# Kernel tuning notes

Measured on AMD Instinct MI355X. Metric: run time of the kernel, lower is better.

## Reference

```python
import jax, jax.numpy as jnp
import numpy as np

B, S, D, H, BLK = 2, 2048, 1024, 16, 128
DH = D // H
NB = S // BLK
EPS = 1e-5
NEG = -1e9


def _make_layout():
    i = np.arange(NB)[:, None]
    j = np.arange(NB)[None, :]
    # causal: local block diagonal + previous block + global first block column
    lay = ((j == i) | (j == i - 1) | (j == 0)) & (j <= i)
    return jnp.asarray(np.broadcast_to(lay, (H, NB, NB)).astype(np.int32))


def setup_inputs() -> dict:
    key = jax.random.key(0)
    ks = jax.random.split(key, 8)
    sd = 1.0 / np.sqrt(D)
    inp = {
        "x": jax.random.normal(ks[0], (B, S, D), jnp.float32),
        "ln1_g": jnp.ones((D,), jnp.float32),
        "ln1_b": jnp.zeros((D,), jnp.float32),
        "Wq": jax.random.normal(ks[1], (D, D), jnp.float32) * sd,
        "bq": jnp.zeros((D,), jnp.float32),
        "Wk": jax.random.normal(ks[2], (D, D), jnp.float32) * sd,
        "bk": jnp.zeros((D,), jnp.float32),
        "Wv": jax.random.normal(ks[3], (D, D), jnp.float32) * sd,
        "bv": jnp.zeros((D,), jnp.float32),
        "Wo": jax.random.normal(ks[4], (D, D), jnp.float32) * sd,
        "bo": jnp.zeros((D,), jnp.float32),
        "ln2_g": jnp.ones((D,), jnp.float32),
        "ln2_b": jnp.zeros((D,), jnp.float32),
        "W1": jax.random.normal(ks[5], (D, 4 * D), jnp.float32) * sd,
        "b1": jnp.zeros((4 * D,), jnp.float32),
        "W2": jax.random.normal(ks[6], (4 * D, D), jnp.float32) * (1.0 / np.sqrt(4 * D)),
        "b2": jnp.zeros((D,), jnp.float32),
        "layout": _make_layout(),
    }
    return inp


def _ln(x, g, b):
    m = jnp.mean(x, -1, keepdims=True)
    v = jnp.var(x, -1, keepdims=True)
    return (x - m) * jax.lax.rsqrt(v + EPS) * g + b


def reference(x, ln1_g, ln1_b, Wq, bq, Wk, bk, Wv, bv, Wo, bo,
              ln2_g, ln2_b, W1, b1, W2, b2, layout):
    # ---- pre-norm block-sparse multi-head attention + residual ----
    h = _ln(x, ln1_g, ln1_b)
    q = (h @ Wq + bq).reshape(B, S, H, DH).transpose(0, 2, 1, 3)
    k = (h @ Wk + bk).reshape(B, S, H, DH).transpose(0, 2, 1, 3)
    v = (h @ Wv + bv).reshape(B, S, H, DH).transpose(0, 2, 1, 3)

    # expand block layout [H,NB,NB] -> token mask [H,S,S], intersect with causal
    blk_mask = jnp.repeat(jnp.repeat(layout > 0, BLK, axis=1), BLK, axis=2)
    causal = jnp.tril(jnp.ones((S, S), bool))
    mask = blk_mask & causal  # [H,S,S]

    scale = DH ** -0.5
    scores = jnp.einsum("bhqd,bhkd->bhqk", q * scale, k)
    scores = jnp.where(mask[None], scores, NEG)
    att = jax.nn.softmax(scores, axis=-1)
    ctx = jnp.einsum("bhqk,bhkd->bhqd", att, v)
    ctx = ctx.transpose(0, 2, 1, 3).reshape(B, S, D)
    x = x + (ctx @ Wo + bo)

    # ---- pre-norm MLP (GeLU) + residual ----
    h2 = _ln(x, ln2_g, ln2_b)
    ff = jax.nn.gelu(h2 @ W1 + b1, approximate=False) @ W2 + b2
    return x + ff
```

## Files before the change

kernel.cpp:

```cpp
#include <hip/hip_runtime.h>

typedef unsigned short ushort;
typedef unsigned int uint;
typedef __attribute__((ext_vector_type(8))) short short8;
typedef __attribute__((ext_vector_type(4))) float floatx4;

#define DEV __device__ __forceinline__

DEV ushort f2bf(float f) {
    uint u = __float_as_uint(f);
    u += 0x7fffu + ((u >> 16) & 1u);
    return (ushort)(u >> 16);
}

DEV void load_lds16(const void* g, const void* l) {
    __builtin_amdgcn_global_load_lds(
        (const __attribute__((address_space(1))) void*)g,
        (__attribute__((address_space(3))) void*)l, 16, 0, 0);
}

template<int ROWS>
DEV void stage_tile(const ushort* g, int ldg, ushort* lds, int w, int lane) {
#pragma unroll
    for (int t = 0; t < ROWS / 32; ++t) {
        int row = t * 32 + w * 8 + (lane >> 3);
        int cg  = (lane & 7) ^ (row & 7);
        load_lds16(g + (size_t)row * ldg + cg * 8, lds + (t * 32 + w * 8) * 64);
    }
}

DEV short8 frag_ld(const ushort* lds, int row, int ks, int quad) {
    int slot = (ks * 4 + quad) ^ (row & 7);
    return *(const short8*)(lds + row * 64 + slot * 8);
}

__global__ __launch_bounds__(256) void transcvt(const float* __restrict__ in,
                                                ushort* __restrict__ out,
                                                int K, int N) {
    __shared__ float t[64][65];
    int tx = threadIdx.x & 63, ty = threadIdx.x >> 6;
    int k0 = blockIdx.y * 64, n0 = blockIdx.x * 64;
#pragma unroll
    for (int r = ty; r < 64; r += 4)
        t[r][tx] = in[(size_t)(k0 + r) * N + n0 + tx];
    __syncthreads();
#pragma unroll
    for (int r = ty; r < 64; r += 4)
        out[(size_t)(n0 + r) * K + k0 + tx] = f2bf(t[tx][r]);
}

__global__ __launch_bounds__(256) void transcvt4(const float* __restrict__ s0,
                                                 const float* __restrict__ s1,
                                                 const float* __restrict__ s2,
                                                 const float* __restrict__ s3,
                                                 ushort* __restrict__ d0,
                                                 ushort* __restrict__ d1,
                                                 ushort* __restrict__ d2,
                                                 ushort* __restrict__ d3) {
    __shared__ float t[64][65];
    int z = blockIdx.z;
    const float* in = z == 0 ? s0 : (z == 1 ? s1 : (z == 2 ? s2 : s3));
    ushort* out     = z == 0 ? d0 : (z == 1 ? d1 : (z == 2 ? d2 : d3));
    int tx = threadIdx.x & 63, ty = threadIdx.x >> 6;
    int k0 = blockIdx.y * 64, n0 = blockIdx.x * 64;
#pragma unroll
    for (int r = ty; r < 64; r += 4)
        t[r][tx] = in[(size_t)(k0 + r) * 1024 + n0 + tx];
    __syncthreads();
#pragma unroll
    for (int r = ty; r < 64; r += 4)
        out[(size_t)(n0 + r) * 1024 + k0 + tx] = f2bf(t[tx][r]);
}

__global__ __launch_bounds__(256) void bias_concat(const float* __restrict__ bq,
                                                   const float* __restrict__ bk,
                                                   const float* __restrict__ bv,
                                                   float* __restrict__ out) {
    int i = blockIdx.x * 256 + threadIdx.x;
    float v = i < 1024 ? bq[i] : (i < 2048 ? bk[i - 1024] : bv[i - 2048]);
    out[i] = v;
}

__global__ __launch_bounds__(256) void ln_kernel(const float* __restrict__ x,
                                                 const float* __restrict__ g,
                                                 const float* __restrict__ bb,
                                                 ushort* __restrict__ out) {
    int row = blockIdx.x, tid = threadIdx.x;
    float4 v = ((const float4*)(x + (size_t)row * 1024))[tid];
    float s = v.x + v.y + v.z + v.w;
    float q = v.x * v.x + v.y * v.y + v.z * v.z + v.w * v.w;
#pragma unroll
    for (int m = 1; m < 64; m <<= 1) {
        s += __shfl_xor(s, m);
        q += __shfl_xor(q, m);
    }
    __shared__ float ss[4], qs[4];
    int w = tid >> 6;
    if ((tid & 63) == 0) { ss[w] = s; qs[w] = q; }
    __syncthreads();
    s = ss[0] + ss[1] + ss[2] + ss[3];
    q = qs[0] + qs[1] + qs[2] + qs[3];
    float mean = s * (1.0f / 1024.0f);
    float var  = q * (1.0f / 1024.0f) - mean * mean;
    float rs   = rsqrtf(var + 1e-5f);
    float4 gv = ((const float4*)g)[tid];
    float4 bv = ((const float4*)bb)[tid];
    ushort o0 = f2bf((v.x - mean) * rs * gv.x + bv.x);
    ushort o1 = f2bf((v.y - mean) * rs * gv.y + bv.y);
    ushort o2 = f2bf((v.z - mean) * rs * gv.z + bv.z);
    ushort o3 = f2bf((v.w - mean) * rs * gv.w + bv.w);
    uint lo = o0 | ((uint)o1 << 16), hi = o2 | ((uint)o3 << 16);
    ((uint2*)(out + (size_t)row * 1024))[tid] = make_uint2(lo, hi);
}

template<int MODE, int JN>
__global__ __launch_bounds__(256) void gemm128(const ushort* __restrict__ A,
                                               const ushort* __restrict__ Bt,
                                               const float* __restrict__ bias,
                                               const float* __restrict__ res,
                                               void* __restrict__ outp,
                                               int M, int N, int K) {
    constexpr int BN = JN * 32;
    __shared__ ushort As[128 * 64];
    __shared__ ushort Bs[BN * 64];
    int tid = threadIdx.x, w = tid >> 6, lane = tid & 63;
    int quad = lane >> 4, l15 = lane & 15;
    int wm = w >> 1, wn = w & 1;
    int m0 = blockIdx.y * 128, n0 = blockIdx.x * BN;

    floatx4 acc[4][JN] = {};
    for (int k0 = 0; k0 < K; k0 += 64) {
        __syncthreads();
        stage_tile<128>(A + (size_t)m0 * K + k0, K, As, w, lane);
        stage_tile<BN>(Bt + (size_t)n0 * K + k0, K, Bs, w, lane);
        __syncthreads();
#pragma unroll
        for (int ks = 0; ks < 2; ++ks) {
            short8 af[4], bfr[JN];
#pragma unroll
            for (int i = 0; i < 4; ++i) af[i] = frag_ld(As, wm * 64 + i * 16 + l15, ks, quad);
#pragma unroll
            for (int j = 0; j < JN; ++j) bfr[j] = frag_ld(Bs, wn * (JN * 16) + j * 16 + l15, ks, quad);
#pragma unroll
            for (int i = 0; i < 4; ++i)
#pragma unroll
                for (int j = 0; j < JN; ++j)
                    acc[i][j] = __builtin_amdgcn_mfma_f32_16x16x32_bf16(af[i], bfr[j], acc[i][j], 0, 0, 0);
        }
    }
#pragma unroll
    for (int j = 0; j < JN; ++j) {
        int col = n0 + wn * (JN * 16) + j * 16 + l15;
        float bv = bias[col];
#pragma unroll
        for (int i = 0; i < 4; ++i) {
#pragma unroll
            for (int r = 0; r < 4; ++r) {
                int row = m0 + wm * 64 + i * 16 + quad * 4 + r;
                float v = acc[i][j][r] + bv;
                if (MODE == 0) {
                    int which = col >> 10, c2 = col & 1023;
                    int b = row >> 11, s = row & 2047, hh = c2 >> 6, dh = c2 & 63;
                    ((ushort*)outp)[(size_t)which * 4194304 +
                                    (((size_t)(b * 16 + hh)) * 2048 + s) * 64 + dh] = f2bf(v);
                } else if (MODE == 1) {
                    float gl = 0.5f * v * (1.0f + erff(v * 0.70710678118f));
                    ((ushort*)outp)[(size_t)row * N + col] = f2bf(gl);
                } else {
                    ((float*)outp)[(size_t)row * N + col] = res[(size_t)row * N + col] + v;
                }
            }
        }
    }
}

__global__ __launch_bounds__(256) void attn_kernel(const ushort* __restrict__ qg,
                                                   const ushort* __restrict__ kg,
                                                   const ushort* __restrict__ vg,
                                                   ushort* __restrict__ ctx) {
    __shared__ ushort Qs[64 * 64];
    __shared__ ushort Ks[128 * 64];
    __shared__ ushort Vs[64 * 136];
    __shared__ ushort Ps[64 * 136];
    int iq2 = blockIdx.x, h = blockIdx.y, b = blockIdx.z;
    int tid = threadIdx.x, w = tid >> 6, lane = tid & 63;
    int quad = lane >> 4, l15 = lane & 15;
    int iq = iq2 >> 1;

    const ushort* qp    = qg + ((size_t)(b * 16 + h) * 2048 + iq2 * 64) * 64;
    const ushort* kbase = kg + (size_t)(b * 16 + h) * 2048 * 64;
    const ushort* vbase = vg + (size_t)(b * 16 + h) * 2048 * 64;

    stage_tile<64>(qp, 64, Qs, w, lane);

    floatx4 o[4] = {};
    float mi[4], li[4];
#pragma unroll
    for (int r = 0; r < 4; ++r) { mi[r] = -1e30f; li[r] = 0.0f; }

    int jbs[3];
    int nj = 0;
    jbs[nj++] = 0;
    if (iq > 1) jbs[nj++] = iq - 1;
    if (iq > 0) jbs[nj++] = iq;

    for (int ji = 0; ji < nj; ++ji) {
        int jb = jbs[ji];
        __syncthreads();
        stage_tile<128>(kbase + (size_t)jb * 128 * 64, 64, Ks, w, lane);
        {
            int dh = tid & 63, sg = tid >> 6;
            const ushort* vp = vbase + (size_t)jb * 128 * 64;
#pragma unroll
            for (int cc = 0; cc < 8; ++cc) {
                int s0 = sg * 32 + cc * 4;
                ushort e0 = vp[(s0 + 0) * 64 + dh];
                ushort e1 = vp[(s0 + 1) * 64 + dh];
                ushort e2 = vp[(s0 + 2) * 64 + dh];
                ushort e3 = vp[(s0 + 3) * 64 + dh];
                uint lo = e0 | ((uint)e1 << 16), hi = e2 | ((uint)e3 << 16);
                *(uint2*)(Vs + dh * 136 + s0) = make_uint2(lo, hi);
            }
        }
        __syncthreads();

        floatx4 sacc[8] = {};
#pragma unroll
        for (int ks = 0; ks < 2; ++ks) {
            short8 af = frag_ld(Qs, w * 16 + l15, ks, quad);
            short8 bf8[8];
#pragma unroll
            for (int nt = 0; nt < 8; ++nt) bf8[nt] = frag_ld(Ks, nt * 16 + l15, ks, quad);
#pragma unroll
            for (int nt = 0; nt < 8; ++nt)
                sacc[nt] = __builtin_amdgcn_mfma_f32_16x16x32_bf16(af, bf8[nt], sacc[nt], 0, 0, 0);
        }

        float rowmax[4] = {-1e30f, -1e30f, -1e30f, -1e30f};
        bool diag = (jb == iq);
        int rowL0 = (iq2 & 1) * 64 + w * 16 + quad * 4;
#pragma unroll
        for (int nt = 0; nt < 8; ++nt) {
#pragma unroll
            for (int r = 0; r < 4; ++r) {
                float xv = sacc[nt][r] * 0.125f;
                if (diag && (nt * 16 + l15 > rowL0 + r)) xv = -1e30f;
                sacc[nt][r] = xv;
                rowmax[r] = fmaxf(rowmax[r], xv);
            }
        }
#pragma unroll
        for (int r = 0; r < 4; ++r)
#pragma unroll
            for (int m = 1; m < 16; m <<= 1)
                rowmax[r] = fmaxf(rowmax[r], __shfl_xor(rowmax[r], m));

        float alpha[4], rsum[4];
#pragma unroll
        for (int r = 0; r < 4; ++r) {
            float mnew = fmaxf(mi[r], rowmax[r]);
            alpha[r] = __expf(mi[r] - mnew);
            mi[r] = mnew;
            rsum[r] = 0.0f;
        }
#pragma unroll
        for (int nt = 0; nt < 8; ++nt) {
#pragma unroll
            for (int r = 0; r < 4; ++r) {
                float p = __expf(sacc[nt][r] - mi[r]);
                rsum[r] += p;
                Ps[(w * 16 + quad * 4 + r) * 136 + nt * 16 + l15] = f2bf(p);
            }
        }
#pragma unroll
        for (int r = 0; r < 4; ++r) {
#pragma unroll
            for (int m = 1; m < 16; m <<= 1) rsum[r] += __shfl_xor(rsum[r], m);
            li[r] = li[r] * alpha[r] + rsum[r];
        }
#pragma unroll
        for (int nt = 0; nt < 4; ++nt)
#pragma unroll
            for (int r = 0; r < 4; ++r) o[nt][r] *= alpha[r];

#pragma unroll
        for (int ks2 = 0; ks2 < 4; ++ks2) {
            short8 ap = *(const short8*)(Ps + (w * 16 + l15) * 136 + ks2 * 32 + quad * 8);
            short8 bv4[4];
#pragma unroll
            for (int nt = 0; nt < 4; ++nt)
                bv4[nt] = *(const short8*)(Vs + (nt * 16 + l15) * 136 + ks2 * 32 + quad * 8);
#pragma unroll
            for (int nt = 0; nt < 4; ++nt)
                o[nt] = __builtin_amdgcn_mfma_f32_16x16x32_bf16(ap, bv4[nt], o[nt], 0, 0, 0);
        }
    }
#pragma unroll
    for (int nt = 0; nt < 4; ++nt) {
#pragma unroll
        for (int r = 0; r < 4; ++r) {
            int srow = iq2 * 64 + w * 16 + quad * 4 + r;
            float val = o[nt][r] / li[r];
            ctx[((size_t)b * 2048 + srow) * 1024 + h * 64 + nt * 16 + l15] = f2bf(val);
        }
    }
}

extern "C" void kernel_launch(void* const* d_in, const int* in_sizes, int n_in,
                              void* d_out, int out_size, void* d_ws, size_t ws_size,
                              hipStream_t stream) {
    (void)in_sizes; (void)n_in; (void)out_size; (void)ws_size;
    const float* x    = (const float*)d_in[0];
    const float* ln1g = (const float*)d_in[1];
    const float* ln1b = (const float*)d_in[2];
    const float* Wq   = (const float*)d_in[3];
    const float* bq   = (const float*)d_in[4];
    const float* Wk   = (const float*)d_in[5];
    const float* bk   = (const float*)d_in[6];
    const float* Wv   = (const float*)d_in[7];
    const float* bv   = (const float*)d_in[8];
    const float* Wo   = (const float*)d_in[9];
    const float* bo   = (const float*)d_in[10];
    const float* ln2g = (const float*)d_in[11];
    const float* ln2b = (const float*)d_in[12];
    const float* W1   = (const float*)d_in[13];
    const float* b1   = (const float*)d_in[14];
    const float* W2   = (const float*)d_in[15];
    const float* b2   = (const float*)d_in[16];

    char* ws = (char*)d_ws;
    size_t off = 0;
    auto alloc = [&](size_t bytes) {
        char* p = ws + off;
        off += (bytes + 255) & ~(size_t)255;
        return p;
    };
    ushort* wqkvT = (ushort*)alloc((size_t)3072 * 1024 * 2);
    ushort* woT   = (ushort*)alloc((size_t)1024 * 1024 * 2);
    ushort* w1T   = (ushort*)alloc((size_t)1024 * 4096 * 2);
    ushort* w2T   = (ushort*)alloc((size_t)4096 * 1024 * 2);
    float*  bqkv  = (float*)alloc((size_t)3072 * 4);
    ushort* hb    = (ushort*)alloc((size_t)4096 * 1024 * 2);
    ushort* qkvb  = (ushort*)alloc((size_t)3 * 4096 * 1024 * 2);
    ushort* ctx   = (ushort*)alloc((size_t)4096 * 1024 * 2);
    float*  x1    = (float*)alloc((size_t)4096 * 1024 * 4);
    ushort* h2    = (ushort*)alloc((size_t)4096 * 1024 * 2);
    ushort* ub    = (ushort*)alloc((size_t)4096 * 4096 * 2);

    transcvt4<<<dim3(16, 16, 4), 256, 0, stream>>>(Wq, Wk, Wv, Wo,
                                                   wqkvT, wqkvT + 1024 * 1024,
                                                   wqkvT + 2048 * 1024, woT);
    transcvt<<<dim3(64, 16), 256, 0, stream>>>(W1, w1T, 1024, 4096);
    transcvt<<<dim3(16, 64), 256, 0, stream>>>(W2, w2T, 4096, 1024);
    bias_concat<<<12, 256, 0, stream>>>(bq, bk, bv, bqkv);

    ln_kernel<<<4096, 256, 0, stream>>>(x, ln1g, ln1b, hb);

    gemm128<0, 4><<<dim3(24, 32), 256, 0, stream>>>(hb, wqkvT, bqkv, nullptr, qkvb,
                                                    4096, 3072, 1024);

    attn_kernel<<<dim3(32, 16, 2), 256, 0, stream>>>(qkvb, qkvb + 3 * 4194304 / 3,
                                                     qkvb + 2 * 4194304, ctx);

    gemm128<2, 2><<<dim3(16, 32), 256, 0, stream>>>(ctx, woT, bo, x, x1, 4096, 1024, 1024);

    ln_kernel<<<4096, 256, 0, stream>>>(x1, ln2g, ln2b, h2);

    gemm128<1, 4><<<dim3(32, 32), 256, 0, stream>>>(h2, w1T, b1, nullptr, ub, 4096, 4096, 1024);
    gemm128<2, 2><<<dim3(16, 32), 256, 0, stream>>>(ub, w2T, b2, x1, (float*)d_out, 4096, 1024, 4096);
}
```

Before: 369.6 us.

## Stage GEMM epilogue through LDS for vector stores, add XCD-aware tile swizzle

The GEMM epilogue now swaps the MFMA operands so each lane holds four consecutive columns, stages the results in shared memory, and writes them out as 16-byte vectorized rows. This replaces the scattered 2-byte and 4-byte per-element stores. Blocks are remapped from a flat grid index so that each XCD works on contiguous 4x4 supertiles, which is meant to improve L2 reuse across chiplets. The four weight-prep kernels are merged into a single launch. The cost is extra LDS round trips and barriers in the epilogue, plus index math that assumes the grid divides evenly across 8 XCDs.

```diff
diff --git a/kernel.cpp b/kernel.cpp
--- a/kernel.cpp
+++ b/kernel.cpp
@@ -34,51 +34,41 @@
     return *(const short8*)(lds + row * 64 + slot * 8);
 }
 
-__global__ __launch_bounds__(256) void transcvt(const float* __restrict__ in,
-                                                ushort* __restrict__ out,
-                                                int K, int N) {
+__global__ __launch_bounds__(256) void prep_kernel(
+    const float* __restrict__ Wq, const float* __restrict__ Wk,
+    const float* __restrict__ Wv, const float* __restrict__ Wo,
+    const float* __restrict__ W1, const float* __restrict__ W2,
+    const float* __restrict__ bq, const float* __restrict__ bk,
+    const float* __restrict__ bv,
+    ushort* __restrict__ wqkvT, ushort* __restrict__ woT,
+    ushort* __restrict__ w1T, ushort* __restrict__ w2T,
+    float* __restrict__ bqkv) {
     __shared__ float t[64][65];
-    int tx = threadIdx.x & 63, ty = threadIdx.x >> 6;
-    int k0 = blockIdx.y * 64, n0 = blockIdx.x * 64;
-#pragma unroll
-    for (int r = ty; r < 64; r += 4)
-        t[r][tx] = in[(size_t)(k0 + r) * N + n0 + tx];
+    int bid = blockIdx.x;
+    const float* in; ushort* out; int K, N, tx, ty;
+    if (bid < 1024) {
+        int m = bid >> 8, r = bid & 255;
+        in  = m == 0 ? Wq : (m == 1 ? Wk : (m == 2 ? Wv : Wo));
+        out = m < 3 ? wqkvT + (size_t)m * 1024 * 1024 : woT;
+        K = 1024; N = 1024; tx = r & 15; ty = r >> 4;
+    } else if (bid < 2048) {
+        int r = bid - 1024; in = W1; out = w1T; K = 1024; N = 4096; tx = r & 63; ty = r >> 6;
+    } else {
+        int r = bid - 2048; in = W2; out = w2T; K = 4096; N = 1024; tx = r & 15; ty = r >> 4;
+    }
+    int txx = threadIdx.x & 63, tyy = threadIdx.x >> 6;
+    int k0 = ty * 64, n0 = tx * 64;
+#pragma unroll
+    for (int r2 = tyy; r2 < 64; r2 += 4)
+        t[r2][txx] = in[(size_t)(k0 + r2) * N + n0 + txx];
     __syncthreads();
 #pragma unroll
-    for (int r = ty; r < 64; r += 4)
-        out[(size_t)(n0 + r) * K + k0 + tx] = f2bf(t[tx][r]);
-}
-
-__global__ __launch_bounds__(256) void transcvt4(const float* __restrict__ s0,
-                                                 const float* __restrict__ s1,
-                                                 const float* __restrict__ s2,
-                                                 const float* __restrict__ s3,
-                                                 ushort* __restrict__ d0,
-                                                 ushort* __restrict__ d1,
-                                                 ushort* __restrict__ d2,
-                                                 ushort* __restrict__ d3) {
-    __shared__ float t[64][65];
-    int z = blockIdx.z;
-    const float* in = z == 0 ? s0 : (z == 1 ? s1 : (z == 2 ? s2 : s3));
-    ushort* out     = z == 0 ? d0 : (z == 1 ? d1 : (z == 2 ? d2 : d3));
-    int tx = threadIdx.x & 63, ty = threadIdx.x >> 6;
-    int k0 = blockIdx.y * 64, n0 = blockIdx.x * 64;
-#pragma unroll
-    for (int r = ty; r < 64; r += 4)
-        t[r][tx] = in[(size_t)(k0 + r) * 1024 + n0 + tx];
-    __syncthreads();
-#pragma unroll
-    for (int r = ty; r < 64; r += 4)
-        out[(size_t)(n0 + r) * 1024 + k0 + tx] = f2bf(t[tx][r]);
-}
-
-__global__ __launch_bounds__(256) void bias_concat(const float* __restrict__ bq,
-                                                   const float* __restrict__ bk,
-                                                   const float* __restrict__ bv,
-                                                   float* __restrict__ out) {
-    int i = blockIdx.x * 256 + threadIdx.x;
-    float v = i < 1024 ? bq[i] : (i < 2048 ? bk[i - 1024] : bv[i - 2048]);
-    out[i] = v;
+    for (int r2 = tyy; r2 < 64; r2 += 4)
+        out[(size_t)(n0 + r2) * K + k0 + txx] = f2bf(t[txx][r2]);
+    if (bid < 12) {
+        int i = bid * 256 + threadIdx.x;
+        bqkv[i] = i < 1024 ? bq[i] : (i < 2048 ? bk[i - 1024] : bv[i - 2048]);
+    }
 }
 
 __global__ __launch_bounds__(256) void ln_kernel(const float* __restrict__ x,
@@ -119,14 +109,23 @@
                                                const float* __restrict__ bias,
                                                const float* __restrict__ res,
                                                void* __restrict__ outp,
-                                               int M, int N, int K) {
+                                               int M, int N, int K,
+                                               int stx_n, int per_xcd) {
     constexpr int BN = JN * 32;
-    __shared__ ushort As[128 * 64];
-    __shared__ ushort Bs[BN * 64];
+    __shared__ ushort smemu[128 * 64 + BN * 64];
+    ushort* As = smemu;
+    ushort* Bs = smemu + 128 * 64;
     int tid = threadIdx.x, w = tid >> 6, lane = tid & 63;
     int quad = lane >> 4, l15 = lane & 15;
     int wm = w >> 1, wn = w & 1;
-    int m0 = blockIdx.y * 128, n0 = blockIdx.x * BN;
+
+    int flat = blockIdx.x;
+    int xcd = flat & 7, slot = flat >> 3;
+    int st = xcd * per_xcd + (slot >> 4);
+    int li = slot & 15;
+    int bx = (st % stx_n) * 4 + (li & 3);
+    int by = (st / stx_n) * 4 + (li >> 2);
+    int m0 = by * 128, n0 = bx * BN;
 
     floatx4 acc[4][JN] = {};
     for (int k0 = 0; k0 < K; k0 += 64) {
@@ -145,30 +144,80 @@
             for (int i = 0; i < 4; ++i)
 #pragma unroll
                 for (int j = 0; j < JN; ++j)
-                    acc[i][j] = __builtin_amdgcn_mfma_f32_16x16x32_bf16(af[i], bfr[j], acc[i][j], 0, 0, 0);
-        }
-    }
-#pragma unroll
-    for (int j = 0; j < JN; ++j) {
-        int col = n0 + wn * (JN * 16) + j * 16 + l15;
-        float bv = bias[col];
-#pragma unroll
-        for (int i = 0; i < 4; ++i) {
-#pragma unroll
-            for (int r = 0; r < 4; ++r) {
-                int row = m0 + wm * 64 + i * 16 + quad * 4 + r;
-                float v = acc[i][j][r] + bv;
-                if (MODE == 0) {
-                    int which = col >> 10, c2 = col & 1023;
-                    int b = row >> 11, s = row & 2047, hh = c2 >> 6, dh = c2 & 63;
-                    ((ushort*)outp)[(size_t)which * 4194304 +
-                                    (((size_t)(b * 16 + hh)) * 2048 + s) * 64 + dh] = f2bf(v);
-                } else if (MODE == 1) {
-                    float gl = 0.5f * v * (1.0f + erff(v * 0.70710678118f));
-                    ((ushort*)outp)[(size_t)row * N + col] = f2bf(gl);
-                } else {
-                    ((float*)outp)[(size_t)row * N + col] = res[(size_t)row * N + col] + v;
+                    acc[i][j] = __builtin_amdgcn_mfma_f32_16x16x32_bf16(bfr[j], af[i], acc[i][j], 0, 0, 0);
+        }
+    }
+
+    ushort* Sb = smemu;
+    float*  Sf = (float*)smemu;
+    int rl  = wm * 16 + l15;
+    int rl2 = tid >> 3, c8 = tid & 7;
+#pragma unroll
+    for (int i = 0; i < 4; ++i) {
+        __syncthreads();
+        if (MODE == 2) {
+#pragma unroll
+            for (int j = 0; j < JN; ++j) {
+                int cbase = wn * (JN * 16) + j * 16 + quad * 4;
+                float4 wv;
+                wv.x = acc[i][j][0]; wv.y = acc[i][j][1];
+                wv.z = acc[i][j][2]; wv.w = acc[i][j][3];
+                *(float4*)(Sf + rl * 68 + cbase) = wv;
+            }
+        } else {
+#pragma unroll
+            for (int j = 0; j < JN; ++j) {
+                int cbase = wn * (JN * 16) + j * 16 + quad * 4;
+                float4 bv4 = *(const float4*)(bias + n0 + cbase);
+                float v0 = acc[i][j][0] + bv4.x, v1 = acc[i][j][1] + bv4.y;
+                float v2 = acc[i][j][2] + bv4.z, v3 = acc[i][j][3] + bv4.w;
+                if (MODE == 1) {
+                    v0 = 0.5f * v0 * (1.0f + erff(v0 * 0.70710678118f));
+                    v1 = 0.5f * v1 * (1.0f + erff(v1 * 0.70710678118f));
+                    v2 = 0.5f * v2 * (1.0f + erff(v2 * 0.70710678118f));
+                    v3 = 0.5f * v3 * (1.0f + erff(v3 * 0.70710678118f));
                 }
+                uint lo = f2bf(v0) | ((uint)f2bf(v1) << 16);
+                uint hi = f2bf(v2) | ((uint)f2bf(v3) << 16);
+                *(uint2*)(Sb + rl * 136 + cbase) = make_uint2(lo, hi);
+            }
+        }
+        __syncthreads();
+        int grow = m0 + (rl2 >> 4) * 64 + i * 16 + (rl2 & 15);
+        if (MODE == 2) {
+            int gc = n0 + c8 * 8;
+            float4 u0 = *(float4*)(Sf + rl2 * 68 + c8 * 8);
+            float4 u1 = *(float4*)(Sf + rl2 * 68 + c8 * 8 + 4);
+            float4 b0 = *(const float4*)(bias + gc);
+            float4 b1 = *(const float4*)(bias + gc + 4);
+            const float* rp = res + (size_t)grow * N + gc;
+            float4 r0 = *(const float4*)rp;
+            float4 r1 = *(const float4*)(rp + 4);
+            float4 o0, o1;
+            o0.x = u0.x + b0.x + r0.x; o0.y = u0.y + b0.y + r0.y;
+            o0.z = u0.z + b0.z + r0.z; o0.w = u0.w + b0.w + r0.w;
+            o1.x = u1.x + b1.x + r1.x; o1.y = u1.y + b1.y + r1.y;
+            o1.z = u1.z + b1.z + r1.z; o1.w = u1.w + b1.w + r1.w;
+            float* op = (float*)outp + (size_t)grow * N + gc;
+            *(float4*)op = o0;
+            *(float4*)(op + 4) = o1;
+        } else {
+            short8 d0 = *(short8*)(Sb + rl2 * 136 + c8 * 8);
+            short8 d1 = *(short8*)(Sb + rl2 * 136 + c8 * 8 + 64);
+            if (MODE == 1) {
+                ushort* op = (ushort*)outp + (size_t)grow * N + n0 + c8 * 8;
+                *(short8*)op = d0;
+                *(short8*)(op + 64) = d1;
+            } else {
+                int b = grow >> 11, s = grow & 2047;
+                int which = n0 >> 10, nbase = n0 & 1023;
+                int h0 = nbase >> 6;
+                size_t b0a = (size_t)which * 4194304 +
+                             (((size_t)(b * 16 + h0)) * 2048 + s) * 64 + c8 * 8;
+                size_t b1a = (size_t)which * 4194304 +
+                             (((size_t)(b * 16 + h0 + 1)) * 2048 + s) * 64 + c8 * 8;
+                *(short8*)((ushort*)outp + b0a) = d0;
+                *(short8*)((ushort*)outp + b1a) = d1;
             }
         }
     }
@@ -347,25 +396,24 @@
     ushort* h2    = (ushort*)alloc((size_t)4096 * 1024 * 2);
     ushort* ub    = (ushort*)alloc((size_t)4096 * 4096 * 2);
 
-    transcvt4<<<dim3(16, 16, 4), 256, 0, stream>>>(Wq, Wk, Wv, Wo,
-                                                   wqkvT, wqkvT + 1024 * 1024,
-                                                   wqkvT + 2048 * 1024, woT);
-    transcvt<<<dim3(64, 16), 256, 0, stream>>>(W1, w1T, 1024, 4096);
-    transcvt<<<dim3(16, 64), 256, 0, stream>>>(W2, w2T, 4096, 1024);
-    bias_concat<<<12, 256, 0, stream>>>(bq, bk, bv, bqkv);
+    prep_kernel<<<3072, 256, 0, stream>>>(Wq, Wk, Wv, Wo, W1, W2, bq, bk, bv,
+                                          wqkvT, woT, w1T, w2T, bqkv);
 
     ln_kernel<<<4096, 256, 0, stream>>>(x, ln1g, ln1b, hb);
 
-    gemm128<0, 4><<<dim3(24, 32), 256, 0, stream>>>(hb, wqkvT, bqkv, nullptr, qkvb,
-                                                    4096, 3072, 1024);
-
-    attn_kernel<<<dim3(32, 16, 2), 256, 0, stream>>>(qkvb, qkvb + 3 * 4194304 / 3,
+    gemm128<0, 4><<<768, 256, 0, stream>>>(hb, wqkvT, bqkv, nullptr, qkvb,
+                                           4096, 3072, 1024, 6, 6);
+
+    attn_kernel<<<dim3(32, 16, 2), 256, 0, stream>>>(qkvb, qkvb + 4194304,
                                                      qkvb + 2 * 4194304, ctx);
 
-    gemm128<2, 2><<<dim3(16, 32), 256, 0, stream>>>(ctx, woT, bo, x, x1, 4096, 1024, 1024);
+    gemm128<2, 2><<<512, 256, 0, stream>>>(ctx, woT, bo, x, x1,
+                                           4096, 1024, 1024, 4, 4);
 
     ln_kernel<<<4096, 256, 0, stream>>>(x1, ln2g, ln2b, h2);
 
-    gemm128<1, 4><<<dim3(32, 32), 256, 0, stream>>>(h2, w1T, b1, nullptr, ub, 4096, 4096, 1024);
-    gemm128<2, 2><<<dim3(16, 32), 256, 0, stream>>>(ub, w2T, b2, x1, (float*)d_out, 4096, 1024, 4096);
-}
+    gemm128<1, 4><<<1024, 256, 0, stream>>>(h2, w1T, b1, nullptr, ub,
+                                            4096, 4096, 1024, 8, 8);
+    gemm128<2, 2><<<512, 256, 0, stream>>>(ub, w2T, b2, x1, (float*)d_out,
+                                           4096, 1024, 4096, 4, 4);
+}
```

Measured after the change: 354.7 us. -4.0%, faster.
